# Performance work log

Measured on AMD Instinct MI355X. Metric: run time of the kernel, lower is better.

## Reference

```python
import jax, jax.numpy as jnp
import numpy as np

B, C, CI, H, W = 8, 256, 128, 64, 64
EPS = 1e-5

def conv1x1(x, w, b):
    # x: [B,C,H,W], w: [O,C], b: [O]
    return jnp.einsum('bchw,oc->bohw', x, w) + b[None, :, None, None]

def avgpool2(x):
    b, c, h, w = x.shape
    return x.reshape(b, c, h // 2, 2, w // 2, 2).mean(axis=(3, 5))

def setup_inputs() -> dict:
    key = jax.random.key(0)
    ks = jax.random.split(key, 16)
    s = lambda fan: 1.0 / np.sqrt(fan)
    inp = {
        'q': jax.random.normal(ks[0], (B, C, H, W), jnp.float32),
        'k': jax.random.normal(ks[1], (B, C, H, W), jnp.float32),
        'v': jax.random.normal(ks[2], (B, C, H, W), jnp.float32),
        'Wg':  jax.random.normal(ks[3], (CI, C), jnp.float32) * s(C),
        'bg':  jax.random.normal(ks[4], (CI,), jnp.float32) * s(C),
        'Wth': jax.random.normal(ks[5], (CI, C), jnp.float32) * s(C),
        'bth': jax.random.normal(ks[6], (CI,), jnp.float32) * s(C),
        'Wph': jax.random.normal(ks[7], (CI, C), jnp.float32) * s(C),
        'bph': jax.random.normal(ks[8], (CI,), jnp.float32) * s(C),
        'Ww':  jax.random.normal(ks[9], (C, CI), jnp.float32) * s(CI),
        'bw':  jax.random.normal(ks[10], (C,), jnp.float32) * s(CI),
        'gamma': jax.random.normal(ks[11], (C,), jnp.float32) * 0.1 + 1.0,
        'beta':  jax.random.normal(ks[12], (C,), jnp.float32) * 0.1,
        'mean':  jax.random.normal(ks[13], (C,), jnp.float32) * 0.1,
        'var':   jax.random.uniform(ks[14], (C,), jnp.float32, 0.5, 1.5),
    }
    return inp

def reference(q, k, v, Wg, bg, Wth, bth, Wph, bph, Ww, bw, gamma, beta, mean, var):
    b = q.shape[0]
    # g branch on v, phi branch on q: 1x1 conv then 2x2 avg-pool (sub_sample)
    g_x = avgpool2(conv1x1(v, Wg, bg)).reshape(b, CI, -1)            # [B,CI,M]
    g_x = g_x.transpose(0, 2, 1)                                      # [B,M,CI]
    theta_x = conv1x1(k, Wth, bth).reshape(b, CI, -1).transpose(0, 2, 1)  # [B,N,CI]
    phi_x = avgpool2(conv1x1(q, Wph, bph)).reshape(b, CI, -1)        # [B,CI,M]
    f = jnp.einsum('bnc,bcm->bnm', theta_x, phi_x)                   # [B,N,M]
    f_div_C = jax.nn.softmax(f, axis=-1)
    y = jnp.einsum('bnm,bmc->bnc', f_div_C, g_x)                     # [B,N,CI]
    y = y.transpose(0, 2, 1).reshape(b, CI, H, W)
    W_y = conv1x1(y, Ww, bw)
    # BatchNorm2d (inference form)
    W_y = (W_y - mean[None, :, None, None]) * (gamma[None, :, None, None]
            * jax.lax.rsqrt(var + EPS)[None, :, None, None]) + beta[None, :, None, None]
    return W_y + v
```

## Files before the change

### kernel.cpp

```cpp
#include <hip/hip_runtime.h>
#include <cstddef>

typedef unsigned short u16;
typedef unsigned int u32;
typedef __attribute__((ext_vector_type(8))) __bf16 bf16x8;
typedef __attribute__((ext_vector_type(4))) float f32x4;

constexpr int kB = 8, kC = 256, kCI = 128, kN = 4096, kM = 1024;
constexpr float kEPS = 1e-5f;

__device__ __forceinline__ u16 f2bf(float f) {
    u32 u = __float_as_uint(f);
    u32 r = (u + 0x7fffu + ((u >> 16) & 1u)) >> 16;
    return (u16)r;
}

__global__ __launch_bounds__(256) void prep_kernel(const float* __restrict__ Wth,
                                                   const float* __restrict__ Wph,
                                                   const float* __restrict__ Wg,
                                                   const float* __restrict__ Ww,
                                                   const float* __restrict__ bw,
                                                   const float* __restrict__ gamma,
                                                   const float* __restrict__ beta,
                                                   const float* __restrict__ mean,
                                                   const float* __restrict__ var,
                                                   u16* __restrict__ Wthb,
                                                   u16* __restrict__ Wphb,
                                                   u16* __restrict__ Wgb,
                                                   u16* __restrict__ Wwsb,
                                                   float* __restrict__ bb) {
    int idx = blockIdx.x * 256 + threadIdx.x;
    if (idx < 32768) {
        Wthb[idx] = f2bf(Wth[idx]);
    } else if (idx < 65536) {
        int j = idx - 32768; Wphb[j] = f2bf(Wph[j]);
    } else if (idx < 98304) {
        int j = idx - 65536; Wgb[j] = f2bf(Wg[j]);
    } else {
        int j = idx - 98304;
        int co = j >> 7;
        float sc = gamma[co] * rsqrtf(var[co] + kEPS);
        Wwsb[j] = f2bf(Ww[j] * sc);
        if ((j & 127) == 0) bb[co] = (bw[co] - mean[co]) * sc + beta[co];
    }
}

template <int POOL>
__device__ __forceinline__ void conv_body(const float* __restrict__ x,
                                          const u16* __restrict__ Wb,
                                          const float* __restrict__ bias,
                                          u16* __restrict__ out, int Mn,
                                          int cmajor, int b, int n0) {
    __shared__ __align__(16) u16 w_lds[128 * 72];
    __shared__ __align__(16) u16 x_lds[64 * 64];
    int t = threadIdx.x;
    int w = t >> 6, lane = t & 63, l15 = lane & 15, quad = lane >> 4;
    int xn = t & 63, cbb = (t >> 6) * 2;

    f32x4 acc[8];
#pragma unroll
    for (int i = 0; i < 8; i++) acc[i] = (f32x4){0.f, 0.f, 0.f, 0.f};

    for (int c0 = 0; c0 < kC; c0 += 64) {
        __syncthreads();
#pragma unroll
        for (int i = 0; i < 4; i++) {
            int u = t + 256 * i;
            int ci = u >> 3, blk = u & 7;
            *(uint4*)&w_lds[ci * 72 + blk * 8] =
                *(const uint4*)&Wb[ci * kC + c0 + blk * 8];
        }
#pragma unroll
        for (int cc = 0; cc < 2; cc++) {
            int cb = cbb + cc;
            float f[8];
            if (POOL) {
                int p = n0 + xn, ph_ = p >> 5, pw_ = p & 31;
#pragma unroll
                for (int j = 0; j < 8; j++) {
                    const float* src = x + ((size_t)(b * kC + c0 + cb * 8 + j) * 64
                                            + 2 * ph_) * 64 + 2 * pw_;
                    float2 a = *(const float2*)src;
                    float2 b2 = *(const float2*)(src + 64);
                    f[j] = 0.25f * (a.x + a.y + b2.x + b2.y);
                }
            } else {
#pragma unroll
                for (int j = 0; j < 8; j++)
                    f[j] = x[(size_t)(b * kC + c0 + cb * 8 + j) * Mn + n0 + xn];
            }
            uint4 pk;
            pk.x = (u32)f2bf(f[0]) | ((u32)f2bf(f[1]) << 16);
            pk.y = (u32)f2bf(f[2]) | ((u32)f2bf(f[3]) << 16);
            pk.z = (u32)f2bf(f[4]) | ((u32)f2bf(f[5]) << 16);
            pk.w = (u32)f2bf(f[6]) | ((u32)f2bf(f[7]) << 16);
            *(uint4*)&x_lds[xn * 64 + ((cb ^ (xn & 7)) * 8)] = pk;
        }
        __syncthreads();

#pragma unroll
        for (int ks = 0; ks < 2; ks++) {
            int px = w * 16 + l15;
            bf16x8 xf = *(const bf16x8*)&x_lds[px * 64 + (((ks * 4 + quad) ^ (px & 7)) * 8)];
#pragma unroll
            for (int ct = 0; ct < 8; ct++) {
                bf16x8 wf = *(const bf16x8*)&w_lds[(ct * 16 + l15) * 72 + ks * 32 + quad * 8];
                if (cmajor)
                    acc[ct] = __builtin_amdgcn_mfma_f32_16x16x32_bf16(xf, wf, acc[ct], 0, 0, 0);
                else
                    acc[ct] = __builtin_amdgcn_mfma_f32_16x16x32_bf16(wf, xf, acc[ct], 0, 0, 0);
            }
        }
    }

    if (cmajor == 0) {
        int px = n0 + w * 16 + l15;
#pragma unroll
        for (int ct = 0; ct < 8; ct++) {
            int ci0 = ct * 16 + quad * 4;
            uint2 pk;
            pk.x = (u32)f2bf(acc[ct][0] + bias[ci0 + 0]) |
                   ((u32)f2bf(acc[ct][1] + bias[ci0 + 1]) << 16);
            pk.y = (u32)f2bf(acc[ct][2] + bias[ci0 + 2]) |
                   ((u32)f2bf(acc[ct][3] + bias[ci0 + 3]) << 16);
            *(uint2*)&out[(size_t)(b * Mn + px) * kCI + ci0] = pk;
        }
    } else {
        int px = n0 + w * 16 + quad * 4;
#pragma unroll
        for (int ct = 0; ct < 8; ct++) {
            int ci = ct * 16 + l15;
            float bs = bias[ci];
            uint2 pk;
            pk.x = (u32)f2bf(acc[ct][0] + bs) | ((u32)f2bf(acc[ct][1] + bs) << 16);
            pk.y = (u32)f2bf(acc[ct][2] + bs) | ((u32)f2bf(acc[ct][3] + bs) << 16);
            *(uint2*)&out[(size_t)(b * kCI + ci) * Mn + px] = pk;
        }
    }
}

__global__ __launch_bounds__(256) void convth_kernel(const float* __restrict__ x,
                                                     const u16* __restrict__ Wb,
                                                     const float* __restrict__ bias,
                                                     u16* __restrict__ out) {
    conv_body<0>(x, Wb, bias, out, kN, 0, blockIdx.y, blockIdx.x * 64);
}

__global__ __launch_bounds__(256) void convpg_kernel(const float* __restrict__ q,
                                                     const float* __restrict__ v,
                                                     const u16* __restrict__ Wph,
                                                     const u16* __restrict__ Wg,
                                                     const float* __restrict__ bph,
                                                     const float* __restrict__ bg,
                                                     u16* __restrict__ phi,
                                                     u16* __restrict__ g) {
    int z = blockIdx.z;
    conv_body<1>(z ? v : q, z ? Wg : Wph, z ? bg : bph, z ? g : phi,
                 kM, z, blockIdx.y, blockIdx.x * 64);
}

__global__ __launch_bounds__(256) void attn_kernel(const u16* __restrict__ theta,
                                                   const u16* __restrict__ phi,
                                                   const u16* __restrict__ g,
                                                   u16* __restrict__ y) {
    __shared__ __align__(16) u16 ph_lds[8192];
    __shared__ __align__(16) u16 g_lds[8192];
    __shared__ __align__(16) u16 p_lds[4096];

    int t = threadIdx.x, b = blockIdx.y, n0 = blockIdx.x * 64;
    int w = t >> 6, lane = t & 63, l15 = lane & 15, quad = lane >> 4;
    int sw = (l15 >> 1) & 3;

    bf16x8 thf[4];
    const u16* thB = theta + ((size_t)(b * kN) + n0 + w * 16 + l15) * kCI;
#pragma unroll
    for (int ks = 0; ks < 4; ks++)
        thf[ks] = *(const bf16x8*)&thB[ks * 32 + quad * 8];

    f32x4 oacc[8];
#pragma unroll
    for (int ct = 0; ct < 8; ct++) oacc[ct] = (f32x4){0.f, 0.f, 0.f, 0.f};
    float m_ = -1e30f, l_ = 0.f;

    const u16* phB = phi + (size_t)b * kM * kCI;
    const u16* gB  = g   + (size_t)b * kCI * kM;
    u16* pw = p_lds + w * 1024;

    for (int c0 = 0; c0 < kM; c0 += 64) {
        __syncthreads();
#pragma unroll
        for (int it = 0; it < 4; it++) {
            int u = t + 256 * it;
            int row = u >> 4, cb = u & 15;
            *(uint4*)&ph_lds[(cb >> 2) * 2048 + row * 32 + (((cb & 3) ^ ((row >> 1) & 3)) * 8)] =
                *(const uint4*)&phB[(size_t)(c0 + row) * kCI + cb * 8];
        }
#pragma unroll
        for (int it = 0; it < 4; it++) {
            int u = t + 256 * it;
            int ci = u >> 3, mb = u & 7;
            *(uint4*)&g_lds[(mb >> 2) * 4096 + ci * 32 + (((mb & 3) ^ ((ci >> 1) & 3)) * 8)] =
                *(const uint4*)&gB[(size_t)ci * kM + c0 + mb * 8];
        }
        __syncthreads();

        f32x4 sacc[4];
#pragma unroll
        for (int mt = 0; mt < 4; mt++) sacc[mt] = (f32x4){0.f, 0.f, 0.f, 0.f};
#pragma unroll
        for (int ks = 0; ks < 4; ks++)
#pragma unroll
            for (int mt = 0; mt < 4; mt++) {
                bf16x8 a = *(const bf16x8*)&ph_lds[ks * 2048 + (mt * 16 + l15) * 32 +
                                                   ((quad ^ sw) * 8)];
                sacc[mt] = __builtin_amdgcn_mfma_f32_16x16x32_bf16(a, thf[ks], sacc[mt], 0, 0, 0);
            }

        float mc = -1e30f;
#pragma unroll
        for (int mt = 0; mt < 4; mt++)
#pragma unroll
            for (int r = 0; r < 4; r++) mc = fmaxf(mc, sacc[mt][r]);
        mc = fmaxf(mc, __shfl_xor(mc, 16, 64));
        mc = fmaxf(mc, __shfl_xor(mc, 32, 64));
        float mn = fmaxf(m_, mc);
        int resc = __any(mn != m_);
        float alpha = __expf(m_ - mn);
        m_ = mn;
        float rs = 0.f;
#pragma unroll
        for (int mt = 0; mt < 4; mt++)
#pragma unroll
            for (int r = 0; r < 4; r++) {
                float p = __expf(sacc[mt][r] - mn);
                sacc[mt][r] = p;
                rs += p;
            }
        rs += __shfl_xor(rs, 16, 64);
        rs += __shfl_xor(rs, 32, 64);
        l_ = l_ * alpha + rs;
        if (resc) {
#pragma unroll
            for (int ct = 0; ct < 8; ct++)
#pragma unroll
                for (int r = 0; r < 4; r++) oacc[ct][r] *= alpha;
        }
#pragma unroll
        for (int mt = 0; mt < 4; mt++)
#pragma unroll
            for (int h = 0; h < 2; h++) {
                u32 d = (u32)f2bf(sacc[mt][2 * h]) | ((u32)f2bf(sacc[mt][2 * h + 1]) << 16);
                int m = mt * 16 + quad * 4 + 2 * h;
                int frag = m >> 5;
                int kblk = ((m >> 3) & 3);
                int j = (quad & 1) * 4 + 2 * h;
                *(u32*)&pw[frag * 512 + l15 * 32 + ((kblk ^ sw) * 8) + j] = d;
            }

#pragma unroll
        for (int ks2 = 0; ks2 < 2; ks2++) {
            bf16x8 bfrag = *(const bf16x8*)&pw[ks2 * 512 + l15 * 32 + ((quad ^ sw) * 8)];
#pragma unroll
            for (int ct = 0; ct < 8; ct++) {
                bf16x8 a = *(const bf16x8*)&g_lds[ks2 * 4096 + (ct * 16 + l15) * 32 +
                                                  ((quad ^ sw) * 8)];
                oacc[ct] = __builtin_amdgcn_mfma_f32_16x16x32_bf16(a, bfrag, oacc[ct], 0, 0, 0);
            }
        }
    }

    float inv = 1.0f / l_;
    int n = n0 + w * 16 + l15;
    u16* yr = y + ((size_t)(b * kN) + n) * kCI + quad * 4;
#pragma unroll
    for (int ct = 0; ct < 8; ct++) {
        uint2 pk;
        pk.x = (u32)f2bf(oacc[ct][0] * inv) | ((u32)f2bf(oacc[ct][1] * inv) << 16);
        pk.y = (u32)f2bf(oacc[ct][2] * inv) | ((u32)f2bf(oacc[ct][3] * inv) << 16);
        *(uint2*)&yr[ct * 16] = pk;
    }
}

__global__ __launch_bounds__(256) void final_kernel(const u16* __restrict__ y,
                                                    const u16* __restrict__ Wws,
                                                    const float* __restrict__ bb,
                                                    const float* __restrict__ v,
                                                    float* __restrict__ out) {
    __shared__ __align__(16) u16 y_lds[64 * 136];
    int t = threadIdx.x, b = blockIdx.y, n0 = blockIdx.x * 64;
    int w = t >> 6, lane = t & 63, l15 = lane & 15, quad = lane >> 4;

#pragma unroll
    for (int i = 0; i < 4; i++) {
        int u = t + 256 * i;
        int row = u >> 4, blk = u & 15;
        *(uint4*)&y_lds[row * 136 + blk * 8] =
            *(const uint4*)&y[(size_t)(b * kN + n0 + row) * kCI + blk * 8];
    }
    __syncthreads();

    bf16x8 af[4];
#pragma unroll
    for (int ks = 0; ks < 4; ks++)
        af[ks] = *(const bf16x8*)&y_lds[(w * 16 + l15) * 136 + ks * 32 + quad * 8];

#pragma unroll
    for (int ct = 0; ct < 16; ct++) {
        f32x4 a = (f32x4){0.f, 0.f, 0.f, 0.f};
#pragma unroll
        for (int ks = 0; ks < 4; ks++) {
            bf16x8 bf = *(const bf16x8*)&Wws[(ct * 16 + l15) * kCI + ks * 32 + quad * 8];
            a = __builtin_amdgcn_mfma_f32_16x16x32_bf16(af[ks], bf, a, 0, 0, 0);
        }
        int co = ct * 16 + l15;
        float bbv = bb[co];
        size_t base = (size_t)(b * kC + co) * kN + n0 + w * 16 + quad * 4;
        float4 vv = *(const float4*)&v[base];
        float4 ov;
        ov.x = a[0] + bbv + vv.x;
        ov.y = a[1] + bbv + vv.y;
        ov.z = a[2] + bbv + vv.z;
        ov.w = a[3] + bbv + vv.w;
        *(float4*)&out[base] = ov;
    }
}

extern "C" void kernel_launch(void* const* d_in, const int* in_sizes, int n_in,
                              void* d_out, int out_size, void* d_ws, size_t ws_size,
                              hipStream_t stream) {
    (void)in_sizes; (void)n_in; (void)out_size; (void)ws_size;
    const float* q     = (const float*)d_in[0];
    const float* k     = (const float*)d_in[1];
    const float* v     = (const float*)d_in[2];
    const float* Wg    = (const float*)d_in[3];
    const float* bg    = (const float*)d_in[4];
    const float* Wth   = (const float*)d_in[5];
    const float* bth   = (const float*)d_in[6];
    const float* Wph   = (const float*)d_in[7];
    const float* bph   = (const float*)d_in[8];
    const float* Ww    = (const float*)d_in[9];
    const float* bw    = (const float*)d_in[10];
    const float* gamma = (const float*)d_in[11];
    const float* beta  = (const float*)d_in[12];
    const float* mean  = (const float*)d_in[13];
    const float* var   = (const float*)d_in[14];
    float* out = (float*)d_out;

    u16* wsu = (u16*)d_ws;
    u16*   theta = wsu;
    u16*   phi   = theta + 4194304;
    u16*   gbuf  = phi + 1048576;
    u16*   ybuf  = gbuf + 1048576;
    u16*   Wthb  = ybuf + 4194304;
    u16*   Wphb  = Wthb + 32768;
    u16*   Wgb   = Wphb + 32768;
    u16*   Wwsb  = Wgb + 32768;
    float* bbuf  = (float*)(Wwsb + 32768);

    prep_kernel<<<dim3(512), 256, 0, stream>>>(Wth, Wph, Wg, Ww, bw, gamma, beta,
                                               mean, var, Wthb, Wphb, Wgb, Wwsb, bbuf);
    convth_kernel<<<dim3(64, 8), 256, 0, stream>>>(k, Wthb, bth, theta);
    convpg_kernel<<<dim3(16, 8, 2), 256, 0, stream>>>(q, v, Wphb, Wgb, bph, bg, phi, gbuf);
    attn_kernel<<<dim3(64, 8), 256, 0, stream>>>(theta, phi, gbuf, ybuf);
    final_kernel<<<dim3(64, 8), 256, 0, stream>>>(ybuf, Wwsb, bbuf, v, out);
}
```

Baseline: 254.2 us.

## Merge conv launches, double-buffer attention tiles, shuffle P fragments, split final blocks

```diff
diff --git a/kernel.cpp b/kernel.cpp
--- a/kernel.cpp
+++ b/kernel.cpp
@@ -50,9 +50,8 @@
                                           const u16* __restrict__ Wb,
                                           const float* __restrict__ bias,
                                           u16* __restrict__ out, int Mn,
-                                          int cmajor, int b, int n0) {
-    __shared__ __align__(16) u16 w_lds[128 * 72];
-    __shared__ __align__(16) u16 x_lds[64 * 64];
+                                          int cmajor, int b, int n0,
+                                          u16* w_lds, u16* x_lds) {
     int t = threadIdx.x;
     int w = t >> 6, lane = t & 63, l15 = lane & 15, quad = lane >> 4;
     int xn = t & 63, cbb = (t >> 6) * 2;
@@ -139,33 +138,35 @@
     }
 }
 
-__global__ __launch_bounds__(256) void convth_kernel(const float* __restrict__ x,
-                                                     const u16* __restrict__ Wb,
-                                                     const float* __restrict__ bias,
-                                                     u16* __restrict__ out) {
-    conv_body<0>(x, Wb, bias, out, kN, 0, blockIdx.y, blockIdx.x * 64);
-}
-
-__global__ __launch_bounds__(256) void convpg_kernel(const float* __restrict__ q,
-                                                     const float* __restrict__ v,
-                                                     const u16* __restrict__ Wph,
-                                                     const u16* __restrict__ Wg,
-                                                     const float* __restrict__ bph,
-                                                     const float* __restrict__ bg,
-                                                     u16* __restrict__ phi,
-                                                     u16* __restrict__ g) {
-    int z = blockIdx.z;
-    conv_body<1>(z ? v : q, z ? Wg : Wph, z ? bg : bph, z ? g : phi,
-                 kM, z, blockIdx.y, blockIdx.x * 64);
+__global__ __launch_bounds__(256) void convs_kernel(const float* __restrict__ kin,
+                                                    const float* __restrict__ qin,
+                                                    const float* __restrict__ vin,
+                                                    const u16* __restrict__ Wthb,
+                                                    const u16* __restrict__ Wphb,
+                                                    const u16* __restrict__ Wgb,
+                                                    const float* __restrict__ bth,
+                                                    const float* __restrict__ bph,
+                                                    const float* __restrict__ bg,
+                                                    u16* __restrict__ theta,
+                                                    u16* __restrict__ phi,
+                                                    u16* __restrict__ g) {
+    __shared__ __align__(16) u16 w_lds[128 * 72];
+    __shared__ __align__(16) u16 x_lds[64 * 64];
+    int bx = blockIdx.x, b = blockIdx.y;
+    if (bx < 64)
+        conv_body<0>(kin, Wthb, bth, theta, kN, 0, b, bx * 64, w_lds, x_lds);
+    else if (bx < 80)
+        conv_body<1>(qin, Wphb, bph, phi, kM, 0, b, (bx - 64) * 64, w_lds, x_lds);
+    else
+        conv_body<1>(vin, Wgb, bg, g, kM, 1, b, (bx - 80) * 64, w_lds, x_lds);
 }
 
 __global__ __launch_bounds__(256) void attn_kernel(const u16* __restrict__ theta,
                                                    const u16* __restrict__ phi,
                                                    const u16* __restrict__ g,
                                                    u16* __restrict__ y) {
-    __shared__ __align__(16) u16 ph_lds[8192];
-    __shared__ __align__(16) u16 g_lds[8192];
-    __shared__ __align__(16) u16 p_lds[4096];
+    __shared__ __align__(16) u16 ph_lds[2 * 8192];
+    __shared__ __align__(16) u16 g_lds[2 * 8192];
 
     int t = threadIdx.x, b = blockIdx.y, n0 = blockIdx.x * 64;
     int w = t >> 6, lane = t & 63, l15 = lane & 15, quad = lane >> 4;
@@ -184,23 +185,34 @@
 
     const u16* phB = phi + (size_t)b * kM * kCI;
     const u16* gB  = g   + (size_t)b * kCI * kM;
-    u16* pw = p_lds + w * 1024;
-
-    for (int c0 = 0; c0 < kM; c0 += 64) {
-        __syncthreads();
+
+    uint4 phr[4], gr[4];
+#pragma unroll
+    for (int it = 0; it < 4; it++) {
+        int u = t + 256 * it;
+        phr[it] = *(const uint4*)&phB[(size_t)(u >> 4) * kCI + (u & 15) * 8];
+        gr[it]  = *(const uint4*)&gB[(size_t)(u >> 3) * kM + (u & 7) * 8];
+    }
+
+    for (int cidx = 0; cidx < 16; cidx++) {
+        u16* phb = ph_lds + (cidx & 1) * 8192;
+        u16* gbL = g_lds + (cidx & 1) * 8192;
 #pragma unroll
         for (int it = 0; it < 4; it++) {
             int u = t + 256 * it;
             int row = u >> 4, cb = u & 15;
-            *(uint4*)&ph_lds[(cb >> 2) * 2048 + row * 32 + (((cb & 3) ^ ((row >> 1) & 3)) * 8)] =
-                *(const uint4*)&phB[(size_t)(c0 + row) * kCI + cb * 8];
-        }
-#pragma unroll
-        for (int it = 0; it < 4; it++) {
-            int u = t + 256 * it;
+            *(uint4*)&phb[(cb >> 2) * 2048 + row * 32 + (((cb & 3) ^ ((row >> 1) & 3)) * 8)] = phr[it];
             int ci = u >> 3, mb = u & 7;
-            *(uint4*)&g_lds[(mb >> 2) * 4096 + ci * 32 + (((mb & 3) ^ ((ci >> 1) & 3)) * 8)] =
-                *(const uint4*)&gB[(size_t)ci * kM + c0 + mb * 8];
+            *(uint4*)&gbL[(mb >> 2) * 4096 + ci * 32 + (((mb & 3) ^ ((ci >> 1) & 3)) * 8)] = gr[it];
+        }
+        if (cidx < 15) {
+            int c0n = (cidx + 1) * 64;
+#pragma unroll
+            for (int it = 0; it < 4; it++) {
+                int u = t + 256 * it;
+                phr[it] = *(const uint4*)&phB[(size_t)(c0n + (u >> 4)) * kCI + (u & 15) * 8];
+                gr[it]  = *(const uint4*)&gB[(size_t)(u >> 3) * kM + c0n + (u & 7) * 8];
+            }
         }
         __syncthreads();
 
@@ -211,8 +223,8 @@
         for (int ks = 0; ks < 4; ks++)
 #pragma unroll
             for (int mt = 0; mt < 4; mt++) {
-                bf16x8 a = *(const bf16x8*)&ph_lds[ks * 2048 + (mt * 16 + l15) * 32 +
-                                                   ((quad ^ sw) * 8)];
+                bf16x8 a = *(const bf16x8*)&phb[ks * 2048 + (mt * 16 + l15) * 32 +
+                                                ((quad ^ sw) * 8)];
                 sacc[mt] = __builtin_amdgcn_mfma_f32_16x16x32_bf16(a, thf[ks], sacc[mt], 0, 0, 0);
             }
 
@@ -245,26 +257,30 @@
 #pragma unroll
                 for (int r = 0; r < 4; r++) oacc[ct][r] *= alpha;
         }
+
+        u32 d[4][2];
 #pragma unroll
         for (int mt = 0; mt < 4; mt++)
 #pragma unroll
-            for (int h = 0; h < 2; h++) {
-                u32 d = (u32)f2bf(sacc[mt][2 * h]) | ((u32)f2bf(sacc[mt][2 * h + 1]) << 16);
-                int m = mt * 16 + quad * 4 + 2 * h;
-                int frag = m >> 5;
-                int kblk = ((m >> 3) & 3);
-                int j = (quad & 1) * 4 + 2 * h;
-                *(u32*)&pw[frag * 512 + l15 * 32 + ((kblk ^ sw) * 8) + j] = d;
-            }
+            for (int h = 0; h < 2; h++)
+                d[mt][h] = (u32)f2bf(sacc[mt][2 * h]) |
+                           ((u32)f2bf(sacc[mt][2 * h + 1]) << 16);
 
 #pragma unroll
         for (int ks2 = 0; ks2 < 2; ks2++) {
-            bf16x8 bfrag = *(const bf16x8*)&pw[ks2 * 512 + l15 * 32 + ((quad ^ sw) * 8)];
+            union { u32 u[4]; bf16x8 v; } bu;
+#pragma unroll
+            for (int jj = 0; jj < 4; jj++) {
+                int srcl = 16 * ((quad & 1) * 2 + (jj >> 1)) + l15;
+                u32 va = (u32)__shfl((int)d[ks2 * 2 + 0][jj & 1], srcl, 64);
+                u32 vb = (u32)__shfl((int)d[ks2 * 2 + 1][jj & 1], srcl, 64);
+                bu.u[jj] = (quad >> 1) ? vb : va;
+            }
 #pragma unroll
             for (int ct = 0; ct < 8; ct++) {
-                bf16x8 a = *(const bf16x8*)&g_lds[ks2 * 4096 + (ct * 16 + l15) * 32 +
-                                                  ((quad ^ sw) * 8)];
-                oacc[ct] = __builtin_amdgcn_mfma_f32_16x16x32_bf16(a, bfrag, oacc[ct], 0, 0, 0);
+                bf16x8 a = *(const bf16x8*)&gbL[ks2 * 4096 + (ct * 16 + l15) * 32 +
+                                                ((quad ^ sw) * 8)];
+                oacc[ct] = __builtin_amdgcn_mfma_f32_16x16x32_bf16(a, bu.v, oacc[ct], 0, 0, 0);
             }
         }
     }
@@ -286,12 +302,12 @@
                                                     const float* __restrict__ bb,
                                                     const float* __restrict__ v,
                                                     float* __restrict__ out) {
-    __shared__ __align__(16) u16 y_lds[64 * 136];
-    int t = threadIdx.x, b = blockIdx.y, n0 = blockIdx.x * 64;
+    __shared__ __align__(16) u16 y_lds[32 * 136];
+    int t = threadIdx.x, b = blockIdx.y, n0 = blockIdx.x * 32;
     int w = t >> 6, lane = t & 63, l15 = lane & 15, quad = lane >> 4;
 
 #pragma unroll
-    for (int i = 0; i < 4; i++) {
+    for (int i = 0; i < 2; i++) {
         int u = t + 256 * i;
         int row = u >> 4, blk = u & 15;
         *(uint4*)&y_lds[row * 136 + blk * 8] =
@@ -299,13 +315,15 @@
     }
     __syncthreads();
 
+    int p = w & 1, coh = (w >> 1) * 8;
     bf16x8 af[4];
 #pragma unroll
     for (int ks = 0; ks < 4; ks++)
-        af[ks] = *(const bf16x8*)&y_lds[(w * 16 + l15) * 136 + ks * 32 + quad * 8];
-
-#pragma unroll
-    for (int ct = 0; ct < 16; ct++) {
+        af[ks] = *(const bf16x8*)&y_lds[(p * 16 + l15) * 136 + ks * 32 + quad * 8];
+
+#pragma unroll
+    for (int ct2 = 0; ct2 < 8; ct2++) {
+        int ct = coh + ct2;
         f32x4 a = (f32x4){0.f, 0.f, 0.f, 0.f};
 #pragma unroll
         for (int ks = 0; ks < 4; ks++) {
@@ -314,7 +332,7 @@
         }
         int co = ct * 16 + l15;
         float bbv = bb[co];
-        size_t base = (size_t)(b * kC + co) * kN + n0 + w * 16 + quad * 4;
+        size_t base = (size_t)(b * kC + co) * kN + n0 + p * 16 + quad * 4;
         float4 vv = *(const float4*)&v[base];
         float4 ov;
         ov.x = a[0] + bbv + vv.x;
@@ -359,8 +377,8 @@
 
     prep_kernel<<<dim3(512), 256, 0, stream>>>(Wth, Wph, Wg, Ww, bw, gamma, beta,
                                                mean, var, Wthb, Wphb, Wgb, Wwsb, bbuf);
-    convth_kernel<<<dim3(64, 8), 256, 0, stream>>>(k, Wthb, bth, theta);
-    convpg_kernel<<<dim3(16, 8, 2), 256, 0, stream>>>(q, v, Wphb, Wgb, bph, bg, phi, gbuf);
+    convs_kernel<<<dim3(96, 8), 256, 0, stream>>>(k, q, v, Wthb, Wphb, Wgb,
+                                                  bth, bph, bg, theta, phi, gbuf);
     attn_kernel<<<dim3(64, 8), 256, 0, stream>>>(theta, phi, gbuf, ybuf);
-    final_kernel<<<dim3(64, 8), 256, 0, stream>>>(ybuf, Wwsb, bbuf, v, out);
-}
+    final_kernel<<<dim3(128, 8), 256, 0, stream>>>(ybuf, Wwsb, bbuf, v, out);
+}
```

Result: slower. 260.3 us (+2.4%).
